# Kernel tuning notes

Hardware: AMD Instinct MI355X
Metric: run time of the kernel (lower is better)

Reference implementation:

```python
import jax, jax.numpy as jnp
import numpy as np

C_S, C_Z, H = 384, 128, 8
HD = C_S // H
EPS = 1e-5

def _layernorm(x, g, b):
    mu = jnp.mean(x, axis=-1, keepdims=True)
    var = jnp.mean((x - mu) ** 2, axis=-1, keepdims=True)
    return (x - mu) * jax.lax.rsqrt(var + EPS) * g + b

def setup_inputs() -> dict:
    key = jax.random.key(0)
    ks = jax.random.split(key, 12)
    B, L = 1, 768
    sc = lambda d: 1.0 / np.sqrt(d)
    return {
        "single": jax.random.normal(ks[0], (B, L, C_S), jnp.float32),
        "pair": jax.random.normal(ks[1], (B, L, L, C_Z), jnp.float32),
        "g_s": jnp.ones((C_S,), jnp.float32),
        "b_s": jnp.zeros((C_S,), jnp.float32),
        "g_z": jnp.ones((C_Z,), jnp.float32),
        "b_z": jnp.zeros((C_Z,), jnp.float32),
        "Wq": jax.random.normal(ks[2], (C_S, C_S), jnp.float32) * sc(C_S),
        "Wk": jax.random.normal(ks[3], (C_S, C_S), jnp.float32) * sc(C_S),
        "Wv": jax.random.normal(ks[4], (C_S, C_S), jnp.float32) * sc(C_S),
        "Wb": jax.random.normal(ks[5], (C_Z, H), jnp.float32) * sc(C_Z),
        "Wo": jax.random.normal(ks[6], (C_S, C_S), jnp.float32) * sc(C_S),
        "bo": jnp.zeros((C_S,), jnp.float32),
        "Wg": jax.random.normal(ks[7], (C_S, C_S), jnp.float32) * sc(C_S),
        "bg": jnp.zeros((C_S,), jnp.float32),
    }

def reference(single, pair, g_s, b_s, g_z, b_z, Wq, Wk, Wv, Wb, Wo, bo, Wg, bg):
    B, L, _ = single.shape
    s = _layernorm(single, g_s, b_s)                      # [B,L,C_S]
    z = _layernorm(pair, g_z, b_z)                        # [B,L,L,C_Z]
    q = (s @ Wq.T).reshape(B, L, H, HD)
    k = (s @ Wk.T).reshape(B, L, H, HD)
    v = (s @ Wv.T).reshape(B, L, H, HD)
    attn = jnp.einsum('bihd,bjhd->bhij', q, k) / np.sqrt(HD)
    bias = jnp.einsum('bijz,zh->bhij', z, Wb)             # pair bias per head
    attn = jax.nn.softmax(attn + bias, axis=-1)
    out = jnp.einsum('bhij,bjhd->bihd', attn, v).reshape(B, L, C_S)
    gate = jax.nn.sigmoid(s @ Wg.T + bg)
    return single + gate * (out @ Wo.T + bo)
```

## Files before the change

kernel.cpp:

```cpp
#include <hip/hip_runtime.h>
#include <hip/hip_bf16.h>
#include <cstdint>
#include <cstddef>

#define LSEQ 768
#define CS 384
#define CZ 128
#define NH 8
#define HD 48
#define LL (LSEQ*LSEQ)

static constexpr float EPS = 1e-5f;
static constexpr float QK_SCALE = 0.14433756729740643f;

__global__ void k_ln_single(const float* __restrict__ single,
                            const float* __restrict__ g,
                            const float* __restrict__ b,
                            float* __restrict__ s_out){
  const int i = blockIdx.x;
  const int lane = threadIdx.x;
  const float* row = single + i*CS;
  float x[6];
  float sum = 0.f;
#pragma unroll
  for(int e=0;e<6;e++){ x[e] = row[lane + 64*e]; sum += x[e]; }
#pragma unroll
  for(int m=32;m>=1;m>>=1) sum += __shfl_xor(sum, m, 64);
  const float mu = sum * (1.f/CS);
  float vs = 0.f;
#pragma unroll
  for(int e=0;e<6;e++){ float d = x[e]-mu; vs += d*d; }
#pragma unroll
  for(int m=32;m>=1;m>>=1) vs += __shfl_xor(vs, m, 64);
  const float rs = rsqrtf(vs*(1.f/CS) + EPS);
#pragma unroll
  for(int e=0;e<6;e++){
    int c = lane + 64*e;
    s_out[i*CS + c] = (x[e]-mu)*rs*g[c] + b[c];
  }
}

__global__ __launch_bounds__(256,4) void k_pair_bias(
    const float* __restrict__ pair,
    const float* __restrict__ g_z,
    const float* __restrict__ b_z,
    const float* __restrict__ Wb,
    float* __restrict__ bias){
  const int t = threadIdx.x;
  const int lane = t & 63;
  const int wave = t >> 6;
  const int sub  = lane >> 4;
  const int lg   = lane & 15;
  const int z0   = lg*8;

  float wb_r[64], gz[8], bz[8];
#pragma unroll
  for(int zz=0; zz<8; zz++){
    gz[zz] = g_z[z0+zz];
    bz[zz] = b_z[z0+zz];
#pragma unroll
    for(int h=0; h<NH; h++) wb_r[zz*8+h] = Wb[(z0+zz)*NH + h];
  }

  const int ngroups = LL/16;
  for(int gidx = blockIdx.x; gidx < ngroups; gidx += gridDim.x){
    const int r = gidx*16 + wave*4 + sub;
    const float4 u0 = *(const float4*)(pair + (size_t)r*CZ + z0);
    const float4 u1 = *(const float4*)(pair + (size_t)r*CZ + z0 + 4);
    float x[8] = {u0.x,u0.y,u0.z,u0.w,u1.x,u1.y,u1.z,u1.w};
    float sum=0.f, sq=0.f;
#pragma unroll
    for(int e=0;e<8;e++){ sum += x[e]; sq += x[e]*x[e]; }
#pragma unroll
    for(int m=1;m<16;m<<=1){ sum += __shfl_xor(sum,m,64); sq += __shfl_xor(sq,m,64); }
    const float mu = sum*(1.f/CZ);
    const float rs = rsqrtf(sq*(1.f/CZ) - mu*mu + EPS);
    float zn[8];
#pragma unroll
    for(int e=0;e<8;e++) zn[e] = (x[e]-mu)*rs*gz[e] + bz[e];
    float acc[8];
#pragma unroll
    for(int h=0;h<8;h++){
      float a = 0.f;
#pragma unroll
      for(int e=0;e<8;e++) a += zn[e]*wb_r[e*8+h];
      acc[h]=a;
    }
#pragma unroll
    for(int h=0;h<8;h++){
#pragma unroll
      for(int m=1;m<16;m<<=1) acc[h] += __shfl_xor(acc[h],m,64);
    }
    float outv = acc[0];
#pragma unroll
    for(int h=1;h<8;h++) if(lg==h) outv = acc[h];
    if(lg < 8) bias[(size_t)lg*LL + r] = outv;
  }
}

__global__ __launch_bounds__(256) void k_qkvg(
    const float* __restrict__ s,
    const float* __restrict__ Wq, const float* __restrict__ Wk,
    const float* __restrict__ Wv, const float* __restrict__ Wg,
    const float* __restrict__ bg,
    float* __restrict__ q, float* __restrict__ k,
    float* __restrict__ v, float* __restrict__ gate){
  const int which = blockIdx.z;
  const float* W = (which==0)?Wq : (which==1)?Wk : (which==2)?Wv : Wg;
  float* out = (which==0)?q : (which==1)?k : (which==2)?v : gate;
  __shared__ float As[16][65];
  __shared__ float Bs[16][65];
  const int t = threadIdx.x;
  const int m0 = blockIdx.x*64;
  const int n0 = blockIdx.y*64;
  const int tx = t & 15, ty = t >> 4;
  float acc[4][4] = {};
  for(int k0=0;k0<CS;k0+=16){
#pragma unroll
    for(int e=0;e<4;e++){
      int idx = t + e*256;
      int kk = idx & 15, mm = idx >> 4;
      As[kk][mm] = s[(m0+mm)*CS + k0 + kk];
      Bs[kk][mm] = W[(n0+mm)*CS + k0 + kk];
    }
    __syncthreads();
#pragma unroll
    for(int kk=0;kk<16;kk++){
      float a[4], bb[4];
#pragma unroll
      for(int rr=0;rr<4;rr++) a[rr]=As[kk][ty+16*rr];
#pragma unroll
      for(int cc=0;cc<4;cc++) bb[cc]=Bs[kk][tx+16*cc];
#pragma unroll
      for(int rr=0;rr<4;rr++)
#pragma unroll
        for(int cc=0;cc<4;cc++) acc[rr][cc] += a[rr]*bb[cc];
    }
    __syncthreads();
  }
#pragma unroll
  for(int rr=0;rr<4;rr++){
    int m = m0 + ty + 16*rr;
#pragma unroll
    for(int cc=0;cc<4;cc++){
      int n = n0 + tx + 16*cc;
      float val = acc[rr][cc];
      if(which==3) val = 1.f/(1.f + __expf(-(val + bg[n])));
      out[m*CS+n] = val;
    }
  }
}

__global__ __launch_bounds__(256) void k_qk(
    const float* __restrict__ q, const float* __restrict__ k,
    float* __restrict__ logits){
  const int h  = blockIdx.z;
  const int i0 = blockIdx.y*32;
  const int j0 = blockIdx.x*64;
  __shared__ float Qs[32][49];
  __shared__ float Ks[64][49];
  const int t = threadIdx.x;
#pragma unroll
  for(int e=0;e<6;e++){
    int idx = t + e*256;
    int d = idx % 48, ii = idx / 48;
    Qs[ii][d] = q[(i0+ii)*CS + h*HD + d];
  }
#pragma unroll
  for(int e=0;e<12;e++){
    int idx = t + e*256;
    int d = idx % 48, jj = idx / 48;
    Ks[jj][d] = k[(j0+jj)*CS + h*HD + d];
  }
  __syncthreads();
  const int tx = t & 15, ty = t >> 4;
  float acc[2][4] = {};
#pragma unroll
  for(int d=0; d<HD; d++){
    float a0 = Qs[ty][d],    a1 = Qs[ty+16][d];
    float b0 = Ks[tx][d],    b1 = Ks[tx+16][d];
    float b2 = Ks[tx+32][d], b3 = Ks[tx+48][d];
    acc[0][0]+=a0*b0; acc[0][1]+=a0*b1; acc[0][2]+=a0*b2; acc[0][3]+=a0*b3;
    acc[1][0]+=a1*b0; acc[1][1]+=a1*b1; acc[1][2]+=a1*b2; acc[1][3]+=a1*b3;
  }
#pragma unroll
  for(int ri=0;ri<2;ri++){
    int i = i0 + ty + 16*ri;
#pragma unroll
    for(int cj=0;cj<4;cj++){
      int j = j0 + tx + 16*cj;
      size_t idx = (size_t)h*LL + (size_t)i*LSEQ + j;
      logits[idx] = acc[ri][cj]*QK_SCALE + logits[idx];
    }
  }
}

__global__ __launch_bounds__(256) void k_softmax(float* __restrict__ logits){
  const int row = blockIdx.x;
  float* p = logits + (size_t)row*LSEQ;
  const int t = threadIdx.x;
  __shared__ float red[4];
  const int wave = t >> 6, lane = t & 63;
  float x[3];
  float mx = -1e30f;
#pragma unroll
  for(int e=0;e<3;e++){ x[e] = p[t + e*256]; mx = fmaxf(mx, x[e]); }
#pragma unroll
  for(int m=32;m>=1;m>>=1) mx = fmaxf(mx, __shfl_xor(mx,m,64));
  if(lane==0) red[wave]=mx;
  __syncthreads();
  mx = fmaxf(fmaxf(red[0],red[1]), fmaxf(red[2],red[3]));
  __syncthreads();
  float sum = 0.f;
#pragma unroll
  for(int e=0;e<3;e++){ x[e] = __expf(x[e]-mx); sum += x[e]; }
#pragma unroll
  for(int m=32;m>=1;m>>=1) sum += __shfl_xor(sum,m,64);
  if(lane==0) red[wave]=sum;
  __syncthreads();
  sum = red[0]+red[1]+red[2]+red[3];
  const float inv = 1.f/sum;
#pragma unroll
  for(int e=0;e<3;e++) p[t+e*256] = x[e]*inv;
}

__global__ __launch_bounds__(256) void k_pv(
    const float* __restrict__ P, const float* __restrict__ v,
    float* __restrict__ attno){
  const int h  = blockIdx.y;
  const int i0 = blockIdx.x*64;
  __shared__ float Ps[64][65];
  __shared__ float Vs[64][49];
  const int t = threadIdx.x;
  const int tx = t & 15, ty = t >> 4;
  float acc[4][3] = {};
  for(int j0=0;j0<LSEQ;j0+=64){
#pragma unroll
    for(int e=0;e<16;e++){
      int idx = t + e*256;
      int jj = idx & 63, ii = idx >> 6;
      Ps[ii][jj] = P[(size_t)h*LL + (size_t)(i0+ii)*LSEQ + j0 + jj];
    }
#pragma unroll
    for(int e=0;e<12;e++){
      int idx = t + e*256;
      int d = idx % 48, jj = idx / 48;
      Vs[jj][d] = v[(j0+jj)*CS + h*HD + d];
    }
    __syncthreads();
#pragma unroll
    for(int jj=0;jj<64;jj++){
      float b0 = Vs[jj][tx], b1 = Vs[jj][tx+16], b2 = Vs[jj][tx+32];
      float a[4];
#pragma unroll
      for(int ri=0;ri<4;ri++) a[ri] = Ps[ty+16*ri][jj];
#pragma unroll
      for(int ri=0;ri<4;ri++){
        acc[ri][0]+=a[ri]*b0; acc[ri][1]+=a[ri]*b1; acc[ri][2]+=a[ri]*b2;
      }
    }
    __syncthreads();
  }
#pragma unroll
  for(int ri=0;ri<4;ri++){
    int i = i0 + ty + 16*ri;
#pragma unroll
    for(int c=0;c<3;c++)
      attno[i*CS + h*HD + tx + 16*c] = acc[ri][c];
  }
}

__global__ __launch_bounds__(256) void k_final(
    const float* __restrict__ attno, const float* __restrict__ Wo,
    const float* __restrict__ bo, const float* __restrict__ single,
    const float* __restrict__ gate, float* __restrict__ out){
  __shared__ float As[16][65];
  __shared__ float Bs[16][65];
  const int t = threadIdx.x;
  const int m0 = blockIdx.x*64;
  const int n0 = blockIdx.y*64;
  const int tx = t & 15, ty = t >> 4;
  float acc[4][4] = {};
  for(int k0=0;k0<CS;k0+=16){
#pragma unroll
    for(int e=0;e<4;e++){
      int idx = t + e*256;
      int kk = idx & 15, mm = idx >> 4;
      As[kk][mm] = attno[(m0+mm)*CS + k0 + kk];
      Bs[kk][mm] = Wo[(n0+mm)*CS + k0 + kk];
    }
    __syncthreads();
#pragma unroll
    for(int kk=0;kk<16;kk++){
      float a[4], bb[4];
#pragma unroll
      for(int rr=0;rr<4;rr++) a[rr]=As[kk][ty+16*rr];
#pragma unroll
      for(int cc=0;cc<4;cc++) bb[cc]=Bs[kk][tx+16*cc];
#pragma unroll
      for(int rr=0;rr<4;rr++)
#pragma unroll
        for(int cc=0;cc<4;cc++) acc[rr][cc] += a[rr]*bb[cc];
    }
    __syncthreads();
  }
#pragma unroll
  for(int rr=0;rr<4;rr++){
    int m = m0 + ty + 16*rr;
#pragma unroll
    for(int cc=0;cc<4;cc++){
      int n = n0 + tx + 16*cc;
      float val = acc[rr][cc] + bo[n];
      out[m*CS+n] = single[m*CS+n] + gate[m*CS+n]*val;
    }
  }
}

extern "C" void kernel_launch(void* const* d_in, const int* in_sizes, int n_in,
                              void* d_out, int out_size, void* d_ws, size_t ws_size,
                              hipStream_t stream){
  (void)in_sizes; (void)n_in; (void)out_size; (void)ws_size;
  const float* single = (const float*)d_in[0];
  const float* pair   = (const float*)d_in[1];
  const float* g_s    = (const float*)d_in[2];
  const float* b_s    = (const float*)d_in[3];
  const float* g_z    = (const float*)d_in[4];
  const float* b_z    = (const float*)d_in[5];
  const float* Wq     = (const float*)d_in[6];
  const float* Wk     = (const float*)d_in[7];
  const float* Wv     = (const float*)d_in[8];
  const float* Wb     = (const float*)d_in[9];
  const float* Wo     = (const float*)d_in[10];
  const float* bo     = (const float*)d_in[11];
  const float* Wg     = (const float*)d_in[12];
  const float* bg     = (const float*)d_in[13];
  float* out = (float*)d_out;

  float* ws     = (float*)d_ws;
  float* logits = ws;
  float* s      = ws + 4718592;
  float* q      = s  + 294912;
  float* k      = q  + 294912;
  float* v      = k  + 294912;
  float* gate   = v  + 294912;
  float* attno  = gate + 294912;

  hipLaunchKernelGGL(k_ln_single, dim3(768),      dim3(64),  0, stream, single, g_s, b_s, s);
  hipLaunchKernelGGL(k_pair_bias, dim3(3072),     dim3(256), 0, stream, pair, g_z, b_z, Wb, logits);
  hipLaunchKernelGGL(k_qkvg,      dim3(12,6,4),   dim3(256), 0, stream, s, Wq, Wk, Wv, Wg, bg, q, k, v, gate);
  hipLaunchKernelGGL(k_qk,        dim3(12,24,8),  dim3(256), 0, stream, q, k, logits);
  hipLaunchKernelGGL(k_softmax,   dim3(6144),     dim3(256), 0, stream, logits);
  hipLaunchKernelGGL(k_pv,        dim3(12,8),     dim3(256), 0, stream, logits, v, attno);
  hipLaunchKernelGGL(k_final,     dim3(12,6),     dim3(256), 0, stream, attno, Wo, bo, single, gate, out);
}
```

Baseline: 584.7 us.

## Fuse QK, softmax and PV into bf16 MFMA flash-attention kernel

Result: faster. 528.4 us (-9.6%).

```diff
diff --git a/kernel.cpp b/kernel.cpp
--- a/kernel.cpp
+++ b/kernel.cpp
@@ -12,6 +12,15 @@
 
 static constexpr float EPS = 1e-5f;
 static constexpr float QK_SCALE = 0.14433756729740643f;
+
+typedef __attribute__((ext_vector_type(8))) short bf16x8;
+typedef __attribute__((ext_vector_type(4))) float f32x4;
+
+__device__ __forceinline__ short f2bf_s(float f){
+  unsigned int u = __float_as_uint(f);
+  unsigned int r = u + 0x7fffu + ((u >> 16) & 1u);
+  return (short)(r >> 16);
+}
 
 __global__ void k_ln_single(const float* __restrict__ single,
                             const float* __restrict__ g,
@@ -61,6 +70,7 @@
 #pragma unroll
     for(int h=0; h<NH; h++) wb_r[zz*8+h] = Wb[(z0+zz)*NH + h];
   }
+  const int hmap = 4*(lg&1) + (lg&2) + ((lg>>2)&1);
 
   const int ngroups = LL/16;
   for(int gidx = blockIdx.x; gidx < ngroups; gidx += gridDim.x){
@@ -75,26 +85,44 @@
     for(int m=1;m<16;m<<=1){ sum += __shfl_xor(sum,m,64); sq += __shfl_xor(sq,m,64); }
     const float mu = sum*(1.f/CZ);
     const float rs = rsqrtf(sq*(1.f/CZ) - mu*mu + EPS);
-    float zn[8];
-#pragma unroll
-    for(int e=0;e<8;e++) zn[e] = (x[e]-mu)*rs*gz[e] + bz[e];
     float acc[8];
 #pragma unroll
-    for(int h=0;h<8;h++){
-      float a = 0.f;
-#pragma unroll
-      for(int e=0;e<8;e++) a += zn[e]*wb_r[e*8+h];
-      acc[h]=a;
-    }
-#pragma unroll
-    for(int h=0;h<8;h++){
-#pragma unroll
-      for(int m=1;m<16;m<<=1) acc[h] += __shfl_xor(acc[h],m,64);
-    }
-    float outv = acc[0];
-#pragma unroll
-    for(int h=1;h<8;h++) if(lg==h) outv = acc[h];
-    if(lg < 8) bias[(size_t)lg*LL + r] = outv;
+    for(int h=0;h<8;h++) acc[h]=0.f;
+#pragma unroll
+    for(int e=0;e<8;e++){
+      const float zn = (x[e]-mu)*rs*gz[e] + bz[e];
+#pragma unroll
+      for(int h=0;h<8;h++) acc[h] += zn*wb_r[e*8+h];
+    }
+    float k1[4];
+    {
+      const bool hi = lg & 1;
+#pragma unroll
+      for(int j=0;j<4;j++){
+        float send = hi ? acc[j] : acc[j+4];
+        float recv = __shfl_xor(send, 1, 64);
+        k1[j] = (hi ? acc[j+4] : acc[j]) + recv;
+      }
+    }
+    float k2[2];
+    {
+      const bool hi = lg & 2;
+#pragma unroll
+      for(int j=0;j<2;j++){
+        float send = hi ? k1[j] : k1[j+2];
+        float recv = __shfl_xor(send, 2, 64);
+        k2[j] = (hi ? k1[j+2] : k1[j]) + recv;
+      }
+    }
+    float k3;
+    {
+      const bool hi = lg & 4;
+      float send = hi ? k2[0] : k2[1];
+      float recv = __shfl_xor(send, 4, 64);
+      k3 = (hi ? k2[1] : k2[0]) + recv;
+    }
+    k3 += __shfl_xor(k3, 8, 64);
+    if(lg < 8) bias[(size_t)hmap*LL + r] = k3;
   }
 }
 
@@ -151,122 +179,146 @@
   }
 }
 
-__global__ __launch_bounds__(256) void k_qk(
+__global__ __launch_bounds__(256) void k_flash(
     const float* __restrict__ q, const float* __restrict__ k,
-    float* __restrict__ logits){
-  const int h  = blockIdx.z;
-  const int i0 = blockIdx.y*32;
-  const int j0 = blockIdx.x*64;
-  __shared__ float Qs[32][49];
-  __shared__ float Ks[64][49];
-  const int t = threadIdx.x;
-#pragma unroll
-  for(int e=0;e<6;e++){
-    int idx = t + e*256;
-    int d = idx % 48, ii = idx / 48;
-    Qs[ii][d] = q[(i0+ii)*CS + h*HD + d];
-  }
-#pragma unroll
-  for(int e=0;e<12;e++){
-    int idx = t + e*256;
-    int d = idx % 48, jj = idx / 48;
-    Ks[jj][d] = k[(j0+jj)*CS + h*HD + d];
-  }
-  __syncthreads();
-  const int tx = t & 15, ty = t >> 4;
-  float acc[2][4] = {};
-#pragma unroll
-  for(int d=0; d<HD; d++){
-    float a0 = Qs[ty][d],    a1 = Qs[ty+16][d];
-    float b0 = Ks[tx][d],    b1 = Ks[tx+16][d];
-    float b2 = Ks[tx+32][d], b3 = Ks[tx+48][d];
-    acc[0][0]+=a0*b0; acc[0][1]+=a0*b1; acc[0][2]+=a0*b2; acc[0][3]+=a0*b3;
-    acc[1][0]+=a1*b0; acc[1][1]+=a1*b1; acc[1][2]+=a1*b2; acc[1][3]+=a1*b3;
-  }
-#pragma unroll
-  for(int ri=0;ri<2;ri++){
-    int i = i0 + ty + 16*ri;
-#pragma unroll
-    for(int cj=0;cj<4;cj++){
-      int j = j0 + tx + 16*cj;
-      size_t idx = (size_t)h*LL + (size_t)i*LSEQ + j;
-      logits[idx] = acc[ri][cj]*QK_SCALE + logits[idx];
-    }
-  }
-}
-
-__global__ __launch_bounds__(256) void k_softmax(float* __restrict__ logits){
-  const int row = blockIdx.x;
-  float* p = logits + (size_t)row*LSEQ;
-  const int t = threadIdx.x;
-  __shared__ float red[4];
-  const int wave = t >> 6, lane = t & 63;
-  float x[3];
-  float mx = -1e30f;
-#pragma unroll
-  for(int e=0;e<3;e++){ x[e] = p[t + e*256]; mx = fmaxf(mx, x[e]); }
-#pragma unroll
-  for(int m=32;m>=1;m>>=1) mx = fmaxf(mx, __shfl_xor(mx,m,64));
-  if(lane==0) red[wave]=mx;
-  __syncthreads();
-  mx = fmaxf(fmaxf(red[0],red[1]), fmaxf(red[2],red[3]));
-  __syncthreads();
-  float sum = 0.f;
-#pragma unroll
-  for(int e=0;e<3;e++){ x[e] = __expf(x[e]-mx); sum += x[e]; }
-#pragma unroll
-  for(int m=32;m>=1;m>>=1) sum += __shfl_xor(sum,m,64);
-  if(lane==0) red[wave]=sum;
-  __syncthreads();
-  sum = red[0]+red[1]+red[2]+red[3];
-  const float inv = 1.f/sum;
-#pragma unroll
-  for(int e=0;e<3;e++) p[t+e*256] = x[e]*inv;
-}
-
-__global__ __launch_bounds__(256) void k_pv(
-    const float* __restrict__ P, const float* __restrict__ v,
+    const float* __restrict__ v, const float* __restrict__ bias,
     float* __restrict__ attno){
   const int h  = blockIdx.y;
-  const int i0 = blockIdx.x*64;
-  __shared__ float Ps[64][65];
-  __shared__ float Vs[64][49];
-  const int t = threadIdx.x;
-  const int tx = t & 15, ty = t >> 4;
-  float acc[4][3] = {};
-  for(int j0=0;j0<LSEQ;j0+=64){
-#pragma unroll
-    for(int e=0;e<16;e++){
-      int idx = t + e*256;
-      int jj = idx & 63, ii = idx >> 6;
-      Ps[ii][jj] = P[(size_t)h*LL + (size_t)(i0+ii)*LSEQ + j0 + jj];
-    }
-#pragma unroll
-    for(int e=0;e<12;e++){
-      int idx = t + e*256;
-      int d = idx % 48, jj = idx / 48;
-      Vs[jj][d] = v[(j0+jj)*CS + h*HD + d];
-    }
-    __syncthreads();
-#pragma unroll
-    for(int jj=0;jj<64;jj++){
-      float b0 = Vs[jj][tx], b1 = Vs[jj][tx+16], b2 = Vs[jj][tx+32];
-      float a[4];
-#pragma unroll
-      for(int ri=0;ri<4;ri++) a[ri] = Ps[ty+16*ri][jj];
-#pragma unroll
-      for(int ri=0;ri<4;ri++){
-        acc[ri][0]+=a[ri]*b0; acc[ri][1]+=a[ri]*b1; acc[ri][2]+=a[ri]*b2;
+  const int i0 = blockIdx.x * 16;
+  const int t  = threadIdx.x;
+  const int w    = t >> 6;
+  const int lane = t & 63;
+  const int ln   = lane & 15;
+  const int quad = lane >> 4;
+
+  __shared__ float S_lds[4][16][34];
+  __shared__ float O_lds[4][16][48];
+  __shared__ float ml_lds[4][2][16];
+
+  bf16x8 aq0, aq1;
+  {
+    const float* qrow = q + (size_t)(i0 + ln)*CS + h*HD;
+#pragma unroll
+    for(int e=0;e<8;e++) aq0[e] = f2bf_s(qrow[quad*8 + e] * QK_SCALE);
+    if(quad < 2){
+#pragma unroll
+      for(int e=0;e<8;e++) aq1[e] = f2bf_s(qrow[32 + quad*8 + e] * QK_SCALE);
+    } else {
+#pragma unroll
+      for(int e=0;e<8;e++) aq1[e] = 0;
+    }
+  }
+
+  float m_r[4], l_r[4];
+  f32x4 o[3];
+#pragma unroll
+  for(int r=0;r<4;r++){ m_r[r] = -INFINITY; l_r[r] = 0.f; }
+#pragma unroll
+  for(int db=0;db<3;db++) o[db] = (f32x4){0.f,0.f,0.f,0.f};
+
+  for(int jt=0; jt<6; jt++){
+    const int j0 = w*192 + jt*32;
+    f32x4 s_f[2];
+#pragma unroll
+    for(int jb=0;jb<2;jb++){
+      const float* krow = k + (size_t)(j0 + jb*16 + ln)*CS + h*HD;
+      bf16x8 bk0, bk1;
+#pragma unroll
+      for(int e=0;e<8;e++) bk0[e] = f2bf_s(krow[quad*8 + e]);
+      if(quad < 2){
+#pragma unroll
+        for(int e=0;e<8;e++) bk1[e] = f2bf_s(krow[32 + quad*8 + e]);
+      } else {
+#pragma unroll
+        for(int e=0;e<8;e++) bk1[e] = 0;
       }
-    }
-    __syncthreads();
-  }
-#pragma unroll
-  for(int ri=0;ri<4;ri++){
-    int i = i0 + ty + 16*ri;
-#pragma unroll
-    for(int c=0;c<3;c++)
-      attno[i*CS + h*HD + tx + 16*c] = acc[ri][c];
+      f32x4 acc = (f32x4){0.f,0.f,0.f,0.f};
+      acc = __builtin_amdgcn_mfma_f32_16x16x32_bf16(aq0, bk0, acc, 0,0,0);
+      acc = __builtin_amdgcn_mfma_f32_16x16x32_bf16(aq1, bk1, acc, 0,0,0);
+      s_f[jb] = acc;
+    }
+    float sv[2][4];
+#pragma unroll
+    for(int jb=0;jb<2;jb++)
+#pragma unroll
+      for(int r=0;r<4;r++)
+        sv[jb][r] = s_f[jb][r] +
+          bias[(size_t)h*LL + (size_t)(i0 + quad*4 + r)*LSEQ + j0 + jb*16 + ln];
+    float tmax[4];
+#pragma unroll
+    for(int r=0;r<4;r++) tmax[r] = fmaxf(sv[0][r], sv[1][r]);
+#pragma unroll
+    for(int r=0;r<4;r++)
+#pragma unroll
+      for(int m=1;m<16;m<<=1) tmax[r] = fmaxf(tmax[r], __shfl_xor(tmax[r], m, 64));
+    float alpha[4];
+#pragma unroll
+    for(int r=0;r<4;r++){
+      const float mn = fmaxf(m_r[r], tmax[r]);
+      alpha[r] = __expf(m_r[r] - mn);
+      m_r[r] = mn;
+    }
+    float p[2][4], tsum[4];
+#pragma unroll
+    for(int r=0;r<4;r++){
+      p[0][r] = __expf(sv[0][r] - m_r[r]);
+      p[1][r] = __expf(sv[1][r] - m_r[r]);
+      tsum[r] = p[0][r] + p[1][r];
+    }
+#pragma unroll
+    for(int r=0;r<4;r++)
+#pragma unroll
+      for(int m=1;m<16;m<<=1) tsum[r] += __shfl_xor(tsum[r], m, 64);
+#pragma unroll
+    for(int r=0;r<4;r++) l_r[r] = l_r[r]*alpha[r] + tsum[r];
+#pragma unroll
+    for(int db=0;db<3;db++)
+#pragma unroll
+      for(int r=0;r<4;r++) o[db][r] *= alpha[r];
+#pragma unroll
+    for(int jb=0;jb<2;jb++)
+#pragma unroll
+      for(int r=0;r<4;r++) S_lds[w][quad*4+r][jb*16+ln] = p[jb][r];
+    bf16x8 ap;
+#pragma unroll
+    for(int e=0;e<8;e++) ap[e] = f2bf_s(S_lds[w][ln][quad*8+e]);
+#pragma unroll
+    for(int db=0;db<3;db++){
+      bf16x8 bv;
+#pragma unroll
+      for(int jj=0;jj<8;jj++)
+        bv[jj] = f2bf_s(v[(size_t)(j0 + quad*8 + jj)*CS + h*HD + db*16 + ln]);
+      o[db] = __builtin_amdgcn_mfma_f32_16x16x32_bf16(ap, bv, o[db], 0,0,0);
+    }
+  }
+
+#pragma unroll
+  for(int db=0;db<3;db++)
+#pragma unroll
+    for(int r=0;r<4;r++) O_lds[w][quad*4+r][db*16+ln] = o[db][r];
+  if(ln == 0){
+#pragma unroll
+    for(int r=0;r<4;r++){
+      ml_lds[w][0][quad*4+r] = m_r[r];
+      ml_lds[w][1][quad*4+r] = l_r[r];
+    }
+  }
+  __syncthreads();
+#pragma unroll
+  for(int e=0;e<3;e++){
+    const int idx = t + e*256;
+    const int row = idx / 48, d = idx % 48;
+    float M = ml_lds[0][0][row];
+#pragma unroll
+    for(int ww=1;ww<4;ww++) M = fmaxf(M, ml_lds[ww][0][row]);
+    float L = 0.f, O = 0.f;
+#pragma unroll
+    for(int ww=0;ww<4;ww++){
+      const float f = __expf(ml_lds[ww][0][row] - M);
+      L += ml_lds[ww][1][row] * f;
+      O += O_lds[ww][row][d] * f;
+    }
+    attno[(size_t)(i0+row)*CS + h*HD + d] = O / L;
   }
 }
 
@@ -337,7 +389,7 @@
   float* out = (float*)d_out;
 
   float* ws     = (float*)d_ws;
-  float* logits = ws;
+  float* bias   = ws;
   float* s      = ws + 4718592;
   float* q      = s  + 294912;
   float* k      = q  + 294912;
@@ -345,11 +397,9 @@
   float* gate   = v  + 294912;
   float* attno  = gate + 294912;
 
-  hipLaunchKernelGGL(k_ln_single, dim3(768),      dim3(64),  0, stream, single, g_s, b_s, s);
-  hipLaunchKernelGGL(k_pair_bias, dim3(3072),     dim3(256), 0, stream, pair, g_z, b_z, Wb, logits);
-  hipLaunchKernelGGL(k_qkvg,      dim3(12,6,4),   dim3(256), 0, stream, s, Wq, Wk, Wv, Wg, bg, q, k, v, gate);
-  hipLaunchKernelGGL(k_qk,        dim3(12,24,8),  dim3(256), 0, stream, q, k, logits);
-  hipLaunchKernelGGL(k_softmax,   dim3(6144),     dim3(256), 0, stream, logits);
-  hipLaunchKernelGGL(k_pv,        dim3(12,8),     dim3(256), 0, stream, logits, v, attno);
-  hipLaunchKernelGGL(k_final,     dim3(12,6),     dim3(256), 0, stream, attno, Wo, bo, single, gate, out);
-}
+  hipLaunchKernelGGL(k_ln_single, dim3(768),     dim3(64),  0, stream, single, g_s, b_s, s);
+  hipLaunchKernelGGL(k_pair_bias, dim3(3072),    dim3(256), 0, stream, pair, g_z, b_z, Wb, bias);
+  hipLaunchKernelGGL(k_qkvg,      dim3(12,6,4),  dim3(256), 0, stream, s, Wq, Wk, Wv, Wg, bg, q, k, v, gate);
+  hipLaunchKernelGGL(k_flash,     dim3(48,8),    dim3(256), 0, stream, q, k, v, bias, attno);
+  hipLaunchKernelGGL(k_final,     dim3(12,6),    dim3(256), 0, stream, attno, Wo, bo, single, gate, out);
+}
```
